# Kernel tuning notes

Hardware: AMD Instinct MI355X
Metric: run time of the kernel (lower is better)

Reference implementation:

```python
import jax, jax.numpy as jnp
import numpy as np

N, IN_DIM, HID, E, NUM_TASKS, TED = 8192, 1024, 2048, 4, 8, 100
MU = 0.01
EPS = 1e-6


def setup_inputs() -> dict:
    key = jax.random.key(0)
    ks = jax.random.split(key, 8)
    s_in = 1.0 / np.sqrt(IN_DIM)
    s_h = 1.0 / np.sqrt(HID)
    return {
        "backbone_output": jax.random.normal(ks[0], (N, IN_DIM), dtype=jnp.float32),
        "task": jax.random.randint(ks[1], (N,), 0, NUM_TASKS),
        "task_embeddings": jax.random.normal(ks[2], (NUM_TASKS, TED), dtype=jnp.float32),
        "routing_matrix": jax.random.normal(ks[3], (IN_DIM + TED, E), dtype=jnp.float32) * 0.05,
        "W1": jax.random.uniform(ks[4], (E, IN_DIM, HID), jnp.float32, -s_in, s_in),
        "b1": jax.random.uniform(ks[5], (E, HID), jnp.float32, -s_in, s_in),
        "W2": jax.random.uniform(ks[6], (E, HID, HID), jnp.float32, -s_h, s_h),
        "b2": jax.random.uniform(ks[7], (E, HID), jnp.float32, -s_h, s_h),
    }


def _gram_schmidt(x):
    # x: [N, E, H] -> orthonormal basis along expert axis via sequential GS
    b0 = x[:, 0] / jnp.linalg.norm(x[:, 0], axis=-1, keepdims=True)
    basis = [b0]
    for i in range(1, x.shape[1]):
        v = x[:, i]                           # [N, H]
        B = jnp.stack(basis, axis=1)          # [N, i, H]
        coef = jnp.einsum("nh,nih->ni", v, B)
        w = v - jnp.einsum("ni,nih->nh", coef, B)
        basis.append(w / jnp.linalg.norm(w, axis=-1, keepdims=True))
    return jnp.stack(basis, axis=1)           # [N, E, H]


def reference(backbone_output, task, task_embeddings, routing_matrix, W1, b1, W2, b2):
    # router: softmax over experts on [x ; task_emb[task]] @ R
    router_in = jnp.concatenate([backbone_output, task_embeddings[task]], axis=-1)
    weights = jax.nn.softmax(router_in @ routing_matrix, axis=-1)   # [N, E]

    # per-expert 2-layer ReLU MLP, all experts at once
    h = jax.nn.relu(jnp.einsum("ni,eih->neh", backbone_output, W1) + b1[None])
    expert_outputs = jax.nn.relu(jnp.einsum("neh,ehk->nek", h, W2) + b2[None])  # [N,E,H]

    # top-1 gate: keep only max weight, zero the rest
    idx = jnp.argmax(weights, axis=-1)
    gates = jnp.where(jnp.arange(weights.shape[-1])[None, :] == idx[:, None], weights, 0.0)

    ortho = _gram_schmidt(expert_outputs)
    tower_input = jnp.einsum("ne,neh->nh", gates, ortho)

    reg_loss = -(1.0 / E) * MU * jnp.sum(jnp.log(gates + EPS), axis=-1)
    return tower_input, reg_loss
```

## Files before the change

### kernel.cpp

```cpp
#include <hip/hip_runtime.h>
#include <hip/hip_bf16.h>
#include <cstdint>

#define N_SAMP 8192
#define IN_DIM 1024
#define HID    2048
#define NE     4

typedef __attribute__((ext_vector_type(8))) __bf16 bf16x8;
typedef __attribute__((ext_vector_type(4))) float  f32x4;

#define MFMA16 __builtin_amdgcn_mfma_f32_16x16x32_bf16

__device__ __forceinline__ unsigned short f2b(float f) {
    unsigned u = __float_as_uint(f);
    u += 0x7fff + ((u >> 16) & 1);
    return (unsigned short)(u >> 16);
}
__device__ __forceinline__ float b2f(unsigned short s) {
    return __uint_as_float(((unsigned)s) << 16);
}

__device__ __forceinline__ void gll16(const void* g, void* l) {
    __builtin_amdgcn_global_load_lds(
        (const __attribute__((address_space(1))) void*)g,
        (__attribute__((address_space(3))) void*)l,
        16, 0, 0);
}

__device__ __forceinline__ int swz(int byte) {
    return byte ^ (((byte >> 7) & 7) << 4);
}

__global__ void conv_bf16(const float* __restrict__ s, unsigned short* __restrict__ d, int n) {
    int i = (blockIdx.x * blockDim.x + threadIdx.x) * 4;
    if (i >= n) return;
    float4 v = *(const float4*)&s[i];
    ushort4 o;
    o.x = f2b(v.x); o.y = f2b(v.y); o.z = f2b(v.z); o.w = f2b(v.w);
    *(ushort4*)&d[i] = o;
}

__global__ void transpose_conv(const float* __restrict__ src, unsigned short* __restrict__ dst,
                               int K, int M) {
    __shared__ float tile[64][65];
    const int k0 = blockIdx.x * 64, m0 = blockIdx.y * 64;
    const int t  = threadIdx.x;
    const int tc = t & 15, tr = t >> 4;
    const float* s = src + (size_t)k0 * M + m0;
    #pragma unroll
    for (int r = tr; r < 64; r += 16) {
        float4 v = *(const float4*)&s[(size_t)r * M + tc * 4];
        tile[r][tc * 4 + 0] = v.x; tile[r][tc * 4 + 1] = v.y;
        tile[r][tc * 4 + 2] = v.z; tile[r][tc * 4 + 3] = v.w;
    }
    __syncthreads();
    unsigned short* d = dst + (size_t)m0 * K + k0;
    #pragma unroll
    for (int r = tr; r < 64; r += 16) {
        ushort4 o;
        o.x = f2b(tile[tc * 4 + 0][r]); o.y = f2b(tile[tc * 4 + 1][r]);
        o.z = f2b(tile[tc * 4 + 2][r]); o.w = f2b(tile[tc * 4 + 3][r]);
        *(ushort4*)&d[(size_t)r * K + tc * 4] = o;
    }
}

__global__ void router_kernel(const float* __restrict__ bb, const int* __restrict__ task,
                              const float* __restrict__ temb, const float* __restrict__ rm,
                              float* __restrict__ gval, int* __restrict__ gidx,
                              float* __restrict__ regout) {
    const int t = threadIdx.x, wave = t >> 6, lane = t & 63;
    const int n = blockIdx.x * 4 + wave;
    const int tk = task[n];
    float a0 = 0.f, a1 = 0.f, a2 = 0.f, a3 = 0.f;
    for (int i = lane; i < IN_DIM + 100; i += 64) {
        float x = (i < IN_DIM) ? bb[(size_t)n * IN_DIM + i] : temb[tk * 100 + (i - IN_DIM)];
        float4 r = *(const float4*)&rm[i * 4];
        a0 += x * r.x; a1 += x * r.y; a2 += x * r.z; a3 += x * r.w;
    }
    #pragma unroll
    for (int o = 32; o; o >>= 1) {
        a0 += __shfl_xor(a0, o); a1 += __shfl_xor(a1, o);
        a2 += __shfl_xor(a2, o); a3 += __shfl_xor(a3, o);
    }
    if (lane == 0) {
        float l[4] = {a0, a1, a2, a3};
        float mx = fmaxf(fmaxf(l[0], l[1]), fmaxf(l[2], l[3]));
        float ex[4], s = 0.f;
        #pragma unroll
        for (int j = 0; j < 4; j++) { ex[j] = expf(l[j] - mx); s += ex[j]; }
        int bi = 0; float bw = ex[0];
        #pragma unroll
        for (int j = 1; j < 4; j++) if (ex[j] > bw) { bw = ex[j]; bi = j; }
        float g = bw / s;
        gval[n] = g;
        gidx[n] = bi;
        regout[n] = -0.0025f * (logf(g + 1e-6f) + 3.0f * logf(1e-6f));
    }
}

__global__ void compact_kernel(const int* __restrict__ gidx, int* __restrict__ list,
                               int* __restrict__ pos, int* __restrict__ cnt) {
    const int e = blockIdx.x;
    const int t = threadIdx.x, lane = t & 63, wave = t >> 6;
    __shared__ int wbase[4];
    __shared__ int running;
    if (t == 0) running = 0;
    __syncthreads();
    int* le = list + (size_t)e * N_SAMP;
    int* pe = pos + (size_t)e * N_SAMP;
    for (int base = 0; base < N_SAMP; base += 256) {
        const int n = base + t;
        const bool f = gidx[n] >= e;
        unsigned long long m = __ballot(f);
        int rank = __popcll(m & ((1ULL << lane) - 1ULL));
        if (lane == 0) wbase[wave] = __popcll(m);
        __syncthreads();
        int wb = 0;
        #pragma unroll
        for (int w = 0; w < 4; w++) if (w < wave) wb += wbase[w];
        int tot = wbase[0] + wbase[1] + wbase[2] + wbase[3];
        int o = running + wb + rank;
        if (f) { le[o] = n; pe[n] = o; }
        __syncthreads();
        if (t == 0) running += tot;
        __syncthreads();
    }
    const int c = running;
    if (t == 0) cnt[e] = c;
    const int padded = (c + 255) & ~255;
    for (int i = c + t; i < padded && i < N_SAMP; i += 256) le[i] = 0;
}

__global__ __launch_bounds__(512, 2) void gemm256(
    const unsigned short* __restrict__ A, const unsigned short* __restrict__ BT,
    const float* __restrict__ bias, unsigned short* __restrict__ C,
    int K, int M, const int* __restrict__ rowlist, const int* __restrict__ cntp) {
    extern __shared__ unsigned short lds_[];
    const int cnt = *cntp;
    const int bid = blockIdx.x;
    const int mb = bid & 7, nb = bid >> 3;
    const int n0 = nb * 256;
    if (n0 >= cnt) return;
    const int m0 = mb * 256;
    const int t = threadIdx.x;
    const int w = t >> 6, lane = t & 63;
    const int wm = w >> 2, wn = w & 3;
    const int lrow = lane & 15, kg = lane >> 4;

    int rr[2], cb[2];
    #pragma unroll
    for (int q = 0; q < 2; q++) {
        int P = (t + q * 512) * 16;
        int Ps = swz(P);
        rr[q] = Ps >> 7;
        cb[q] = Ps & 127;
    }
    int gA[2][2], gB[2][2];
    #pragma unroll
    for (int h = 0; h < 2; h++)
        #pragma unroll
        for (int q = 0; q < 2; q++) {
            int r = n0 + h * 128 + rr[q];
            gA[h][q] = rowlist ? rowlist[r] : r;
            gB[h][q] = m0 + h * 128 + rr[q];
        }

    auto stageA = [&](int buf, int h, int kt) {
        #pragma unroll
        for (int q = 0; q < 2; q++) {
            const char* src = (const char*)(A + (size_t)gA[h][q] * K) + kt * 128 + cb[q];
            gll16(src, &lds_[buf * 32768 + h * 8192 + q * 4096 + w * 512]);
        }
    };
    auto stageB = [&](int buf, int h, int kt) {
        #pragma unroll
        for (int q = 0; q < 2; q++) {
            const char* src = (const char*)(BT + (size_t)gB[h][q] * K) + kt * 128 + cb[q];
            gll16(src, &lds_[buf * 32768 + 16384 + h * 8192 + q * 4096 + w * 512]);
        }
    };
    auto ldA = [&](int buf, int i, int kk) -> bf16x8 {
        int byte = (i * 16 + lrow) * 128 + (kk * 32 + kg * 8) * 2;
        byte = swz(byte);
        return *(const bf16x8*)&lds_[buf * 32768 + wm * 8192 + (byte >> 1)];
    };
    auto ldB = [&](int buf, int j, int kk) -> bf16x8 {
        int byte = ((wn & 1) * 64 + j * 16 + lrow) * 128 + (kk * 32 + kg * 8) * 2;
        byte = swz(byte);
        return *(const bf16x8*)&lds_[buf * 32768 + 16384 + (wn >> 1) * 8192 + (byte >> 1)];
    };

    f32x4 acc[8][4];
    #pragma unroll
    for (int i = 0; i < 8; i++)
        #pragma unroll
        for (int j = 0; j < 4; j++) acc[i][j] = (f32x4){0.f, 0.f, 0.f, 0.f};

    const int nt = K >> 6;

    stageA(0, 0, 0); stageA(0, 1, 0); stageB(0, 0, 0); stageB(0, 1, 0);
    stageA(1, 0, 1); stageA(1, 1, 1); stageB(1, 0, 1);
    asm volatile("s_waitcnt vmcnt(6)" ::: "memory");
    __builtin_amdgcn_s_barrier();

    bf16x8 af[8][2], bf[2][2];
    for (int kt = 0; kt < nt; ++kt) {
        const int buf = kt & 1;
        #pragma unroll
        for (int i = 0; i < 4; i++) { af[i][0] = ldA(buf, i, 0); af[i][1] = ldA(buf, i, 1); }
        #pragma unroll
        for (int j = 0; j < 2; j++) { bf[j][0] = ldB(buf, j, 0); bf[j][1] = ldB(buf, j, 1); }
        if (kt + 1 < nt) stageB(buf ^ 1, 1, kt + 1);
        __builtin_amdgcn_s_barrier();
        __builtin_amdgcn_s_setprio(1);
        #pragma unroll
        for (int i = 0; i < 4; i++)
            #pragma unroll
            for (int j = 0; j < 2; j++) {
                acc[i][j] = MFMA16(af[i][0], bf[j][0], acc[i][j], 0, 0, 0);
                acc[i][j] = MFMA16(af[i][1], bf[j][1], acc[i][j], 0, 0, 0);
            }
        __builtin_amdgcn_s_setprio(0);
        __builtin_amdgcn_s_barrier();
        #pragma unroll
        for (int i = 4; i < 8; i++) { af[i][0] = ldA(buf, i, 0); af[i][1] = ldA(buf, i, 1); }
        __builtin_amdgcn_s_barrier();
        __builtin_amdgcn_s_setprio(1);
        #pragma unroll
        for (int i = 4; i < 8; i++)
            #pragma unroll
            for (int j = 0; j < 2; j++) {
                acc[i][j] = MFMA16(af[i][0], bf[j][0], acc[i][j], 0, 0, 0);
                acc[i][j] = MFMA16(af[i][1], bf[j][1], acc[i][j], 0, 0, 0);
            }
        __builtin_amdgcn_s_setprio(0);
        __builtin_amdgcn_s_barrier();
        #pragma unroll
        for (int j = 0; j < 2; j++) { bf[j][0] = ldB(buf, 2 + j, 0); bf[j][1] = ldB(buf, 2 + j, 1); }
        if (kt + 2 < nt) { stageA(buf, 0, kt + 2); stageA(buf, 1, kt + 2); }
        __builtin_amdgcn_s_barrier();
        __builtin_amdgcn_s_setprio(1);
        #pragma unroll
        for (int i = 0; i < 4; i++)
            #pragma unroll
            for (int j = 0; j < 2; j++) {
                acc[i][2 + j] = MFMA16(af[i][0], bf[j][0], acc[i][2 + j], 0, 0, 0);
                acc[i][2 + j] = MFMA16(af[i][1], bf[j][1], acc[i][2 + j], 0, 0, 0);
            }
        __builtin_amdgcn_s_setprio(0);
        __builtin_amdgcn_s_barrier();
        if (kt + 2 < nt) stageB(buf, 0, kt + 2);
        __builtin_amdgcn_s_barrier();
        __builtin_amdgcn_s_setprio(1);
        #pragma unroll
        for (int i = 4; i < 8; i++)
            #pragma unroll
            for (int j = 0; j < 2; j++) {
                acc[i][2 + j] = MFMA16(af[i][0], bf[j][0], acc[i][2 + j], 0, 0, 0);
                acc[i][2 + j] = MFMA16(af[i][1], bf[j][1], acc[i][2 + j], 0, 0, 0);
            }
        __builtin_amdgcn_s_setprio(0);
        if (kt < nt - 2) asm volatile("s_waitcnt vmcnt(6)" ::: "memory");
        else             asm volatile("s_waitcnt vmcnt(0)" ::: "memory");
        __builtin_amdgcn_s_barrier();
    }

    float bv[4];
    #pragma unroll
    for (int j = 0; j < 4; j++)
        bv[j] = bias[m0 + wn * 64 + j * 16 + lrow];
    #pragma unroll
    for (int i = 0; i < 8; i++) {
        const int srow0 = n0 + wm * 128 + i * 16 + kg * 4;
        #pragma unroll
        for (int j = 0; j < 4; j++) {
            const int col = m0 + wn * 64 + j * 16 + lrow;
            #pragma unroll
            for (int q = 0; q < 4; q++) {
                if (srow0 + q < cnt) {
                    float x = acc[i][j][q] + bv[j];
                    C[(size_t)(srow0 + q) * M + col] = f2b(fmaxf(x, 0.f));
                }
            }
        }
    }
}

__global__ void gs_kernel(const unsigned short* __restrict__ eo, const float* __restrict__ gval,
                          const int* __restrict__ gidx, const int* __restrict__ pos,
                          float* __restrict__ dout) {
    const int t = threadIdx.x, wave = t >> 6, lane = t & 63;
    const int n = blockIdx.x * 4 + wave;
    const int idx = gidx[n];
    const float g = gval[n];

    float v[32], b0[32], b1[32], b2[32];

    auto loadv = [&](float* dst, int e) {
        const size_t row = pos[(size_t)e * N_SAMP + n];
        const unsigned short* p = eo + ((size_t)e * N_SAMP + row) * HID + lane * 8;
        #pragma unroll
        for (int c = 0; c < 4; c++) {
            uint4 u = *(const uint4*)(p + c * 512);
            const unsigned short* us = (const unsigned short*)&u;
            #pragma unroll
            for (int j = 0; j < 8; j++) dst[c * 8 + j] = b2f(us[j]);
        }
    };
    auto wdot = [&](const float* x, const float* y) -> float {
        float s = 0.f;
        #pragma unroll
        for (int k = 0; k < 32; k++) s += x[k] * y[k];
        #pragma unroll
        for (int o = 32; o; o >>= 1) s += __shfl_xor(s, o);
        return s;
    };
    auto storev = [&](const float* b) {
        float* o = dout + (size_t)n * HID + lane * 8;
        #pragma unroll
        for (int c = 0; c < 4; c++) {
            float4 x0, x1;
            x0.x = g * b[c * 8 + 0]; x0.y = g * b[c * 8 + 1];
            x0.z = g * b[c * 8 + 2]; x0.w = g * b[c * 8 + 3];
            x1.x = g * b[c * 8 + 4]; x1.y = g * b[c * 8 + 5];
            x1.z = g * b[c * 8 + 6]; x1.w = g * b[c * 8 + 7];
            *(float4*)(o + c * 512) = x0;
            *(float4*)(o + c * 512 + 4) = x1;
        }
    };

    loadv(v, 0);
    float inv = 1.f / sqrtf(wdot(v, v));
    #pragma unroll
    for (int k = 0; k < 32; k++) b0[k] = v[k] * inv;
    if (idx == 0) { storev(b0); return; }
    loadv(v, 1);
    {
        float cc0 = wdot(v, b0);
        #pragma unroll
        for (int k = 0; k < 32; k++) v[k] -= cc0 * b0[k];
        inv = 1.f / sqrtf(wdot(v, v));
        #pragma unroll
        for (int k = 0; k < 32; k++) b1[k] = v[k] * inv;
    }
    if (idx == 1) { storev(b1); return; }
    loadv(v, 2);
    {
        float cc0 = wdot(v, b0);
        float cc1 = wdot(v, b1);
        #pragma unroll
        for (int k = 0; k < 32; k++) v[k] -= cc0 * b0[k] + cc1 * b1[k];
        inv = 1.f / sqrtf(wdot(v, v));
        #pragma unroll
        for (int k = 0; k < 32; k++) b2[k] = v[k] * inv;
    }
    if (idx == 2) { storev(b2); return; }
    loadv(v, 3);
    {
        float cc0 = wdot(v, b0);
        float cc1 = wdot(v, b1);
        float cc2 = wdot(v, b2);
        #pragma unroll
        for (int k = 0; k < 32; k++) v[k] -= cc0 * b0[k] + cc1 * b1[k] + cc2 * b2[k];
        inv = 1.f / sqrtf(wdot(v, v));
        #pragma unroll
        for (int k = 0; k < 32; k++) v[k] *= inv;
    }
    storev(v);
}

extern "C" void kernel_launch(void* const* d_in, const int* in_sizes, int n_in,
                              void* d_out, int out_size, void* d_ws, size_t ws_size,
                              hipStream_t stream) {
    const float* bb   = (const float*)d_in[0];
    const int*   task = (const int*)d_in[1];
    const float* temb = (const float*)d_in[2];
    const float* rm   = (const float*)d_in[3];
    const float* W1   = (const float*)d_in[4];
    const float* b1   = (const float*)d_in[5];
    const float* W2   = (const float*)d_in[6];
    const float* b2   = (const float*)d_in[7];
    float* out = (float*)d_out;

    char* ws = (char*)d_ws;
    unsigned short* obf  = (unsigned short*)(ws + 0);
    unsigned short* Abf  = (unsigned short*)(ws + 134217728);
    unsigned short* hbf  = (unsigned short*)(ws + 150994944);
    unsigned short* W1T  = (unsigned short*)(ws + 184549376);
    unsigned short* W2T  = (unsigned short*)(ws + 188743680);
    float*          gv   = (float*)(ws + 197132288);
    int*            gi   = (int*)(ws + 197165056);
    int*            list = (int*)(ws + 197197824);
    int*            pos  = (int*)(ws + 197328896);
    int*            cnt  = (int*)(ws + 197459968);

    conv_bf16<<<(N_SAMP * IN_DIM) / 1024, 256, 0, stream>>>(bb, Abf, N_SAMP * IN_DIM);
    router_kernel<<<N_SAMP / 4, 256, 0, stream>>>(bb, task, temb, rm, gv, gi,
                                                  out + (size_t)N_SAMP * HID);
    compact_kernel<<<NE, 256, 0, stream>>>(gi, list, pos, cnt);

    const int gemm_blocks = (HID / 256) * (N_SAMP / 256);
    const size_t lds_bytes = 131072;
    for (int e = 0; e < NE; ++e) {
        transpose_conv<<<dim3(IN_DIM / 64, HID / 64), 256, 0, stream>>>(
            W1 + (size_t)e * IN_DIM * HID, W1T, IN_DIM, HID);
        gemm256<<<gemm_blocks, 512, lds_bytes, stream>>>(
            Abf, W1T, b1 + (size_t)e * HID, hbf, IN_DIM, HID,
            list + (size_t)e * N_SAMP, cnt + e);
        transpose_conv<<<dim3(HID / 64, HID / 64), 256, 0, stream>>>(
            W2 + (size_t)e * HID * HID, W2T, HID, HID);
        gemm256<<<gemm_blocks, 512, lds_bytes, stream>>>(
            hbf, W2T, b2 + (size_t)e * HID, obf + (size_t)e * N_SAMP * HID, HID, HID,
            nullptr, cnt + e);
    }

    gs_kernel<<<N_SAMP / 4, 256, 0, stream>>>(obf, gv, gi, pos, out);
}
```

Baseline: 565.7 us.

## Batch all experts into single grouped GEMM and transpose launches

Weight transposes and both expert GEMM layers now process all four experts in one launch each, indexing the expert from the block id, instead of a per-expert loop of launches. Since each expert only receives a fraction of rows and most blocks exit early, batching is meant to fill the GPU with concurrently active blocks and remove launch serialization. It requires a larger workspace with per-expert hidden and transposed-weight buffers, and falls back to the old sequential path when the workspace is too small.

```diff
diff --git a/kernel.cpp b/kernel.cpp
--- a/kernel.cpp
+++ b/kernel.cpp
@@ -42,12 +42,13 @@
 }
 
 __global__ void transpose_conv(const float* __restrict__ src, unsigned short* __restrict__ dst,
-                               int K, int M) {
+                               int K, int M, size_t srcStride, size_t dstStride) {
     __shared__ float tile[64][65];
+    const int e  = blockIdx.z;
     const int k0 = blockIdx.x * 64, m0 = blockIdx.y * 64;
     const int t  = threadIdx.x;
     const int tc = t & 15, tr = t >> 4;
-    const float* s = src + (size_t)k0 * M + m0;
+    const float* s = src + (size_t)e * srcStride + (size_t)k0 * M + m0;
     #pragma unroll
     for (int r = tr; r < 64; r += 16) {
         float4 v = *(const float4*)&s[(size_t)r * M + tc * 4];
@@ -55,7 +56,7 @@
         tile[r][tc * 4 + 2] = v.z; tile[r][tc * 4 + 3] = v.w;
     }
     __syncthreads();
-    unsigned short* d = dst + (size_t)m0 * K + k0;
+    unsigned short* d = dst + (size_t)e * dstStride + (size_t)m0 * K + k0;
     #pragma unroll
     for (int r = tr; r < 64; r += 16) {
         ushort4 o;
@@ -135,14 +136,23 @@
 __global__ __launch_bounds__(512, 2) void gemm256(
     const unsigned short* __restrict__ A, const unsigned short* __restrict__ BT,
     const float* __restrict__ bias, unsigned short* __restrict__ C,
-    int K, int M, const int* __restrict__ rowlist, const int* __restrict__ cntp) {
+    int K, int M, const int* __restrict__ rowlistBase, const int* __restrict__ cntBase,
+    size_t aStride, size_t btStride, size_t cStride, int listStride) {
     extern __shared__ unsigned short lds_[];
-    const int cnt = *cntp;
     const int bid = blockIdx.x;
-    const int mb = bid & 7, nb = bid >> 3;
+    const int e = bid >> 8;
+    const int inner = bid & 255;
+    const int mb = inner & 7, nb = inner >> 3;
+    const int cnt = cntBase[e];
     const int n0 = nb * 256;
     if (n0 >= cnt) return;
     const int m0 = mb * 256;
+    const unsigned short* Ae  = A + (size_t)e * aStride;
+    const unsigned short* BTe = BT + (size_t)e * btStride;
+    const float*          be  = bias + (size_t)e * HID;
+    unsigned short*       Ce  = C + (size_t)e * cStride;
+    const int* rowlist = listStride ? rowlistBase + (size_t)e * listStride : rowlistBase;
+
     const int t = threadIdx.x;
     const int w = t >> 6, lane = t & 63;
     const int wm = w >> 2, wn = w & 3;
@@ -169,14 +179,14 @@
     auto stageA = [&](int buf, int h, int kt) {
         #pragma unroll
         for (int q = 0; q < 2; q++) {
-            const char* src = (const char*)(A + (size_t)gA[h][q] * K) + kt * 128 + cb[q];
+            const char* src = (const char*)(Ae + (size_t)gA[h][q] * K) + kt * 128 + cb[q];
             gll16(src, &lds_[buf * 32768 + h * 8192 + q * 4096 + w * 512]);
         }
     };
     auto stageB = [&](int buf, int h, int kt) {
         #pragma unroll
         for (int q = 0; q < 2; q++) {
-            const char* src = (const char*)(BT + (size_t)gB[h][q] * K) + kt * 128 + cb[q];
+            const char* src = (const char*)(BTe + (size_t)gB[h][q] * K) + kt * 128 + cb[q];
             gll16(src, &lds_[buf * 32768 + 16384 + h * 8192 + q * 4096 + w * 512]);
         }
     };
@@ -269,7 +279,7 @@
     float bv[4];
     #pragma unroll
     for (int j = 0; j < 4; j++)
-        bv[j] = bias[m0 + wn * 64 + j * 16 + lrow];
+        bv[j] = be[m0 + wn * 64 + j * 16 + lrow];
     #pragma unroll
     for (int i = 0; i < 8; i++) {
         const int srow0 = n0 + wm * 128 + i * 16 + kg * 4;
@@ -280,7 +290,7 @@
             for (int q = 0; q < 4; q++) {
                 if (srow0 + q < cnt) {
                     float x = acc[i][j][q] + bv[j];
-                    C[(size_t)(srow0 + q) * M + col] = f2b(fmaxf(x, 0.f));
+                    Ce[(size_t)(srow0 + q) * M + col] = f2b(fmaxf(x, 0.f));
                 }
             }
         }
@@ -382,38 +392,67 @@
     const float* W2   = (const float*)d_in[6];
     const float* b2   = (const float*)d_in[7];
     float* out = (float*)d_out;
-
     char* ws = (char*)d_ws;
-    unsigned short* obf  = (unsigned short*)(ws + 0);
-    unsigned short* Abf  = (unsigned short*)(ws + 134217728);
-    unsigned short* hbf  = (unsigned short*)(ws + 150994944);
-    unsigned short* W1T  = (unsigned short*)(ws + 184549376);
-    unsigned short* W2T  = (unsigned short*)(ws + 188743680);
-    float*          gv   = (float*)(ws + 197132288);
-    int*            gi   = (int*)(ws + 197165056);
-    int*            list = (int*)(ws + 197197824);
-    int*            pos  = (int*)(ws + 197328896);
-    int*            cnt  = (int*)(ws + 197459968);
-
-    conv_bf16<<<(N_SAMP * IN_DIM) / 1024, 256, 0, stream>>>(bb, Abf, N_SAMP * IN_DIM);
-    router_kernel<<<N_SAMP / 4, 256, 0, stream>>>(bb, task, temb, rm, gv, gi,
-                                                  out + (size_t)N_SAMP * HID);
-    compact_kernel<<<NE, 256, 0, stream>>>(gi, list, pos, cnt);
-
-    const int gemm_blocks = (HID / 256) * (N_SAMP / 256);
+
     const size_t lds_bytes = 131072;
-    for (int e = 0; e < NE; ++e) {
-        transpose_conv<<<dim3(IN_DIM / 64, HID / 64), 256, 0, stream>>>(
-            W1 + (size_t)e * IN_DIM * HID, W1T, IN_DIM, HID);
-        gemm256<<<gemm_blocks, 512, lds_bytes, stream>>>(
-            Abf, W1T, b1 + (size_t)e * HID, hbf, IN_DIM, HID,
-            list + (size_t)e * N_SAMP, cnt + e);
-        transpose_conv<<<dim3(HID / 64, HID / 64), 256, 0, stream>>>(
-            W2 + (size_t)e * HID * HID, W2T, HID, HID);
-        gemm256<<<gemm_blocks, 512, lds_bytes, stream>>>(
-            hbf, W2T, b2 + (size_t)e * HID, obf + (size_t)e * N_SAMP * HID, HID, HID,
-            nullptr, cnt + e);
-    }
-
-    gs_kernel<<<N_SAMP / 4, 256, 0, stream>>>(obf, gv, gi, pos, out);
-}
+    const size_t FUSED_NEED = 302317584;
+
+    if (ws_size >= FUSED_NEED) {
+        unsigned short* hbf  = (unsigned short*)(ws + 0);
+        unsigned short* Abf  = (unsigned short*)(ws + 134217728);
+        unsigned short* W1T  = (unsigned short*)(ws + 150994944);
+        unsigned short* obf  = (unsigned short*)(ws + 134217728);
+        unsigned short* W2T  = (unsigned short*)(ws + 268435456);
+        float*          gv   = (float*)(ws + 301989888);
+        int*            gi   = (int*)(ws + 301989888 + 32768);
+        int*            list = (int*)(ws + 301989888 + 65536);
+        int*            pos  = (int*)(ws + 301989888 + 196608);
+        int*            cnt  = (int*)(ws + 301989888 + 327680);
+
+        conv_bf16<<<(N_SAMP * IN_DIM) / 1024, 256, 0, stream>>>(bb, Abf, N_SAMP * IN_DIM);
+        router_kernel<<<N_SAMP / 4, 256, 0, stream>>>(bb, task, temb, rm, gv, gi,
+                                                      out + (size_t)N_SAMP * HID);
+        compact_kernel<<<NE, 256, 0, stream>>>(gi, list, pos, cnt);
+        transpose_conv<<<dim3(IN_DIM / 64, HID / 64, NE), 256, 0, stream>>>(
+            W1, W1T, IN_DIM, HID, (size_t)IN_DIM * HID, (size_t)IN_DIM * HID);
+        transpose_conv<<<dim3(HID / 64, HID / 64, NE), 256, 0, stream>>>(
+            W2, W2T, HID, HID, (size_t)HID * HID, (size_t)HID * HID);
+        gemm256<<<NE * 256, 512, lds_bytes, stream>>>(
+            Abf, W1T, b1, hbf, IN_DIM, HID, list, cnt,
+            (size_t)0, (size_t)HID * IN_DIM, (size_t)N_SAMP * HID, N_SAMP);
+        gemm256<<<NE * 256, 512, lds_bytes, stream>>>(
+            hbf, W2T, b2, obf, HID, HID, nullptr, cnt,
+            (size_t)N_SAMP * HID, (size_t)HID * HID, (size_t)N_SAMP * HID, 0);
+        gs_kernel<<<N_SAMP / 4, 256, 0, stream>>>(obf, gv, gi, pos, out);
+    } else {
+        unsigned short* obf  = (unsigned short*)(ws + 0);
+        unsigned short* Abf  = (unsigned short*)(ws + 134217728);
+        unsigned short* hbf  = (unsigned short*)(ws + 150994944);
+        unsigned short* W1T  = (unsigned short*)(ws + 184549376);
+        unsigned short* W2T  = (unsigned short*)(ws + 188743680);
+        float*          gv   = (float*)(ws + 197132288);
+        int*            gi   = (int*)(ws + 197165056);
+        int*            list = (int*)(ws + 197197824);
+        int*            pos  = (int*)(ws + 197328896);
+        int*            cnt  = (int*)(ws + 197459968);
+
+        conv_bf16<<<(N_SAMP * IN_DIM) / 1024, 256, 0, stream>>>(bb, Abf, N_SAMP * IN_DIM);
+        router_kernel<<<N_SAMP / 4, 256, 0, stream>>>(bb, task, temb, rm, gv, gi,
+                                                      out + (size_t)N_SAMP * HID);
+        compact_kernel<<<NE, 256, 0, stream>>>(gi, list, pos, cnt);
+
+        for (int e = 0; e < NE; ++e) {
+            transpose_conv<<<dim3(IN_DIM / 64, HID / 64, 1), 256, 0, stream>>>(
+                W1 + (size_t)e * IN_DIM * HID, W1T, IN_DIM, HID, 0, 0);
+            gemm256<<<256, 512, lds_bytes, stream>>>(
+                Abf, W1T, b1 + (size_t)e * HID - (size_t)0 * HID, hbf, IN_DIM, HID,
+                list + (size_t)e * N_SAMP, cnt + e, 0, 0, 0, 0);
+            transpose_conv<<<dim3(HID / 64, HID / 64, 1), 256, 0, stream>>>(
+                W2 + (size_t)e * HID * HID, W2T, HID, HID, 0, 0);
+            gemm256<<<256, 512, lds_bytes, stream>>>(
+                hbf, W2T, b2 + (size_t)e * HID, obf + (size_t)e * N_SAMP * HID, HID, HID,
+                nullptr, cnt + e, 0, 0, 0, 0);
+        }
+        gs_kernel<<<N_SAMP / 4, 256, 0, stream>>>(obf, gv, gi, pos, out);
+    }
+}
```

Result: slower. 627.2 us (+10.9%).
